# Optimization experiments

Measured on AMD Instinct MI355X. Metric: run time of the kernel, lower is better.

The kernel has to match this reference:

```python
import jax, jax.numpy as jnp
import numpy as np

H = 2048            # hidden_size
INTER = 8192        # intermediate_size
E = 16              # num_experts
V = 32000           # vocab_size
I = INTER // E      # per-expert intermediate (tp_size=1) = 512
N = 4096            # num_tokens
BASE_ROUTING_SCALE = 10.0


def setup_inputs() -> dict:
    key = jax.random.key(0)
    ks = jax.random.split(key, 6)
    x = jax.random.normal(ks[0], (N, H), dtype=jnp.float32)
    token_ids = jax.random.randint(ks[1], (N,), 0, V)
    mu = jax.random.normal(ks[2], (N, H), dtype=jnp.float32)
    # kaiming-uniform-ish scaled params
    gate_up_proj = jax.random.normal(ks[3], (E, H, 2 * I), dtype=jnp.float32) * (1.0 / np.sqrt(H))
    down_proj = jax.random.normal(ks[4], (E, I, H), dtype=jnp.float32) * (1.0 / np.sqrt(I))
    # mu_router initialized to zeros in the module; use small random so routing is actually mu-biased
    mu_router_w = jax.random.normal(ks[5], (E, H), dtype=jnp.float32) * 0.02
    return {"x": x, "token_ids": token_ids, "mu": mu,
            "gate_up_proj": gate_up_proj, "down_proj": down_proj,
            "mu_router_w": mu_router_w}


def reference(x, token_ids, mu, gate_up_proj, down_proj, mu_router_w):
    # --- routing: expert = token_id % E, biased by mu logits ---
    base = jnp.clip(token_ids, 0, V - 1) % E              # [N]
    logits = (jax.nn.one_hot(base, E, dtype=jnp.float32) * BASE_ROUTING_SCALE
              + mu @ mu_router_w.T)                       # [N, E]
    expert_ids = jnp.argmax(logits, axis=-1)              # [N]

    Iloc = gate_up_proj.shape[-1] // 2

    # --- grouped expert SwiGLU MLP: scan over experts, mask-combine outputs ---
    def step(acc, inp):
        wg, wd, e = inp
        gu = x @ wg                                       # [N, 2I]
        h = jax.nn.silu(gu[:, :Iloc]) * gu[:, Iloc:]      # [N, I]
        o = h @ wd                                        # [N, H]
        acc = acc + jnp.where((expert_ids == e)[:, None], o, 0.0)
        return acc, None

    out0 = jnp.zeros_like(x)
    out, _ = jax.lax.scan(step, out0, (gate_up_proj, down_proj, jnp.arange(E)))
    return out
```

## Files before the change

kernel.cpp:

```cpp
#include <hip/hip_runtime.h>
#include <hip/hip_bf16.h>

#define NT 4096
#define HD 2048
#define NE 16
#define ID 512
#define TWO_I 1024
#define PITCH 72
#define MAXITEMS 47

typedef __attribute__((ext_vector_type(8))) short bf16x8_t;
typedef __attribute__((ext_vector_type(4))) float f32x4_t;

__device__ __forceinline__ unsigned short f2bf(float f) {
  union { float f; unsigned int u; } v; v.f = f;
  unsigned int r = v.u + 0x7fffu + ((v.u >> 16) & 1u);
  return (unsigned short)(r >> 16);
}
__device__ __forceinline__ unsigned pk2(unsigned short a, unsigned short b) {
  return (unsigned)a | ((unsigned)b << 16);
}
__device__ __forceinline__ void gl_lds16(const void* g, void* l) {
  __builtin_amdgcn_global_load_lds(
      (const __attribute__((address_space(1))) unsigned int*)g,
      (__attribute__((address_space(3))) unsigned int*)l, 16, 0, 0);
}

__global__ void k_cast_x(const float* __restrict__ x, unsigned short* __restrict__ xb) {
  size_t i = ((size_t)blockIdx.x * 256 + threadIdx.x) * 8;
  float4 a = *(const float4*)(x + i);
  float4 b = *(const float4*)(x + i + 4);
  uint4 pk;
  pk.x = pk2(f2bf(a.x), f2bf(a.y)); pk.y = pk2(f2bf(a.z), f2bf(a.w));
  pk.z = pk2(f2bf(b.x), f2bf(b.y)); pk.w = pk2(f2bf(b.z), f2bf(b.w));
  *(uint4*)(xb + i) = pk;
}

__global__ void k_route(const float* __restrict__ mu, const int* __restrict__ tok,
                        const float* __restrict__ wr, int* __restrict__ eid) {
  int t = blockIdx.x;
  int tid = threadIdx.x;
  float p[NE];
#pragma unroll
  for (int e = 0; e < NE; ++e) p[e] = 0.f;
  const float* m = mu + (size_t)t * HD;
  for (int h = tid; h < HD; h += 256) {
    float mv = m[h];
#pragma unroll
    for (int e = 0; e < NE; ++e) p[e] += mv * wr[e * HD + h];
  }
#pragma unroll
  for (int e = 0; e < NE; ++e) {
    float v = p[e];
#pragma unroll
    for (int s = 32; s; s >>= 1) v += __shfl_xor(v, s, 64);
    p[e] = v;
  }
  __shared__ float red[4][NE];
  int lane = tid & 63, wv = tid >> 6;
  if (lane == 0) {
#pragma unroll
    for (int e = 0; e < NE; ++e) red[wv][e] = p[e];
  }
  __syncthreads();
  if (tid == 0) {
    int tk = tok[t];
    if (tk < 0) tk = 0;
    if (tk > 31999) tk = 31999;
    int base = tk & 15;
    float best = -3.0e38f; int bi = 0;
    for (int e = 0; e < NE; ++e) {
      float v = red[0][e] + red[1][e] + red[2][e] + red[3][e];
      if (e == base) v += 10.0f;
      if (v > best) { best = v; bi = e; }
    }
    eid[t] = bi;
  }
}

__global__ void k_init(int* counts, int* cursors) {
  int i = threadIdx.x;
  if (i < NE) { counts[i] = 0; cursors[i] = 0; }
}
__global__ void k_hist(const int* __restrict__ eid, int* __restrict__ counts) {
  int t = blockIdx.x * 256 + threadIdx.x;
  if (t < NT) atomicAdd(&counts[eid[t]], 1);
}
__global__ void k_scan(const int* __restrict__ counts, int* __restrict__ offsets,
                       int* __restrict__ cursors, int* __restrict__ wk) {
  if (threadIdx.x == 0) {
    int s = 0;
    for (int e = 0; e < NE; ++e) { offsets[e] = s; cursors[e] = s; s += counts[e]; }
    offsets[NE] = s;
    int n = 0;
    for (int e = 0; e < NE; ++e) {
      int tiles = (counts[e] + 127) >> 7;
      for (int m = 0; m < tiles; ++m) { wk[n++] = e | (m << 8); }
    }
    wk[MAXITEMS] = n;
  }
}
__global__ void k_scatter(const int* __restrict__ eid, int* __restrict__ cursors,
                          int* __restrict__ tlist) {
  int t = blockIdx.x * 256 + threadIdx.x;
  if (t < NT) {
    int e = eid[t];
    int pos = atomicAdd(&cursors[e], 1);
    tlist[pos] = t;
  }
}

__global__ __launch_bounds__(256, 3) void k_gemm1(
    const unsigned short* __restrict__ xb, const float* __restrict__ gup,
    const int* __restrict__ offsets, const int* __restrict__ tlist,
    const int* __restrict__ wk, unsigned short* __restrict__ hbuf) {
  int item = blockIdx.y;
  if (item >= wk[MAXITEMS]) return;
  int w = wk[item];
  int e = w & 255, tb = (w >> 8) * 128;
  int off = offsets[e], cnt = offsets[e + 1] - off;
  int c0 = blockIdx.x * 32;

  __shared__ float Bbuf[2][64 * 64];
  __shared__ unsigned short Pbuf[2][64 * PITCH];
  __shared__ int ltok[128];

  int tid = threadIdx.x, lane = tid & 63, wv = tid >> 6;
  if (tid < 128) { int r = tb + tid; if (r > cnt - 1) r = cnt - 1; ltok[tid] = tlist[off + r]; }
  __syncthreads();

  int lr = lane & 15, hi = lane >> 4, mb = wv * 32;
  const unsigned short* aRow0 = xb + (size_t)ltok[mb + lr] * HD + hi * 8;
  const unsigned short* aRow1 = xb + (size_t)ltok[mb + 16 + lr] * HD + hi * 8;

  const float* bSrc[4];
  int bDst[4];
  {
    int cc = lane & 15;
    int gcol = (cc < 8) ? (c0 + cc * 4) : (ID + c0 + (cc - 8) * 4);
    const float* Wg = gup + (size_t)e * HD * TWO_I;
#pragma unroll
    for (int i = 0; i < 4; ++i) {
      int kr = wv * 16 + i * 4 + (lane >> 4);
      bSrc[i] = Wg + (size_t)kr * TWO_I + gcol;
      bDst[i] = (wv * 16 + i * 4) * 64;
    }
  }

#define STAGEB(BUF) do { \
  _Pragma("unroll") for (int i = 0; i < 4; ++i) { \
    gl_lds16(bSrc[i], &Bbuf[BUF][bDst[i]]); bSrc[i] += (size_t)64 * TWO_I; } \
} while (0)

  bf16x8_t A0[4], A1[4];
#define LOADA(SET, KT) do { \
  SET[0] = *(const bf16x8_t*)(aRow0 + (KT) * 64); \
  SET[1] = *(const bf16x8_t*)(aRow0 + (KT) * 64 + 32); \
  SET[2] = *(const bf16x8_t*)(aRow1 + (KT) * 64); \
  SET[3] = *(const bf16x8_t*)(aRow1 + (KT) * 64 + 32); \
} while (0)

#define TRANSP(BUF) do { \
  const float* s_ = &Bbuf[BUF][(wv * 16) * 64 + lane]; \
  unsigned short t_[16]; \
  _Pragma("unroll") for (int j = 0; j < 16; ++j) t_[j] = f2bf(s_[j * 64]); \
  uint4 q0_, q1_; \
  q0_.x = pk2(t_[0], t_[1]);   q0_.y = pk2(t_[2], t_[3]); \
  q0_.z = pk2(t_[4], t_[5]);   q0_.w = pk2(t_[6], t_[7]); \
  q1_.x = pk2(t_[8], t_[9]);   q1_.y = pk2(t_[10], t_[11]); \
  q1_.z = pk2(t_[12], t_[13]); q1_.w = pk2(t_[14], t_[15]); \
  *(uint4*)&Pbuf[BUF][lane * PITCH + wv * 16] = q0_; \
  *(uint4*)&Pbuf[BUF][lane * PITCH + wv * 16 + 8] = q1_; \
} while (0)

  f32x4_t zero = {0.f, 0.f, 0.f, 0.f};
  f32x4_t accg[2][2], accu[2][2];
#pragma unroll
  for (int m = 0; m < 2; ++m)
#pragma unroll
    for (int n = 0; n < 2; ++n) { accg[m][n] = zero; accu[m][n] = zero; }

#define MFMA_PH(BUF, SET) do { \
  __builtin_amdgcn_s_setprio(1); \
  _Pragma("unroll") for (int kk = 0; kk < 2; ++kk) { \
    int klo = kk * 32 + hi * 8; \
    bf16x8_t bg0 = *(bf16x8_t*)&Pbuf[BUF][(lr) * PITCH + klo]; \
    bf16x8_t bg1 = *(bf16x8_t*)&Pbuf[BUF][(16 + lr) * PITCH + klo]; \
    bf16x8_t bu0 = *(bf16x8_t*)&Pbuf[BUF][(32 + lr) * PITCH + klo]; \
    bf16x8_t bu1 = *(bf16x8_t*)&Pbuf[BUF][(48 + lr) * PITCH + klo]; \
    bf16x8_t a0 = SET[kk], a1 = SET[2 + kk]; \
    accg[0][0] = __builtin_amdgcn_mfma_f32_16x16x32_bf16(a0, bg0, accg[0][0], 0, 0, 0); \
    accg[0][1] = __builtin_amdgcn_mfma_f32_16x16x32_bf16(a0, bg1, accg[0][1], 0, 0, 0); \
    accu[0][0] = __builtin_amdgcn_mfma_f32_16x16x32_bf16(a0, bu0, accu[0][0], 0, 0, 0); \
    accu[0][1] = __builtin_amdgcn_mfma_f32_16x16x32_bf16(a0, bu1, accu[0][1], 0, 0, 0); \
    accg[1][0] = __builtin_amdgcn_mfma_f32_16x16x32_bf16(a1, bg0, accg[1][0], 0, 0, 0); \
    accg[1][1] = __builtin_amdgcn_mfma_f32_16x16x32_bf16(a1, bg1, accg[1][1], 0, 0, 0); \
    accu[1][0] = __builtin_amdgcn_mfma_f32_16x16x32_bf16(a1, bu0, accu[1][0], 0, 0, 0); \
    accu[1][1] = __builtin_amdgcn_mfma_f32_16x16x32_bf16(a1, bu1, accu[1][1], 0, 0, 0); \
  } \
  __builtin_amdgcn_s_setprio(0); \
} while (0)

#define SUBSTEP(KT, BUF, SET, VMC) do { \
  asm volatile("s_waitcnt vmcnt(" #VMC ")" ::: "memory"); \
  __builtin_amdgcn_sched_barrier(0); \
  TRANSP(BUF); \
  asm volatile("s_waitcnt lgkmcnt(0)" ::: "memory"); \
  __builtin_amdgcn_sched_barrier(0); \
  __builtin_amdgcn_s_barrier(); \
  MFMA_PH(BUF, SET); \
  if ((KT) + 2 < 32) { LOADA(SET, (KT) + 2); STAGEB(BUF); } \
} while (0)

  LOADA(A0, 0); STAGEB(0);
  LOADA(A1, 1); STAGEB(1);

  for (int kt2 = 0; kt2 < 15; ++kt2) {
    SUBSTEP(2 * kt2, 0, A0, 8);
    SUBSTEP(2 * kt2 + 1, 1, A1, 8);
  }
  SUBSTEP(30, 0, A0, 8);
  SUBSTEP(31, 1, A1, 0);

#undef SUBSTEP
#undef MFMA_PH
#undef TRANSP
#undef LOADA
#undef STAGEB

  int rq = hi * 4;
#pragma unroll
  for (int m = 0; m < 2; ++m)
#pragma unroll
    for (int n = 0; n < 2; ++n)
#pragma unroll
      for (int j = 0; j < 4; ++j) {
        int r = tb + mb + m * 16 + rq + j;
        if (r < cnt) {
          float g = accg[m][n][j], u = accu[m][n][j];
          float hv = (g / (1.f + __expf(-g))) * u;
          hbuf[(size_t)(off + r) * ID + c0 + n * 16 + lr] = f2bf(hv);
        }
      }
}

__global__ __launch_bounds__(256, 3) void k_gemm2(
    const unsigned short* __restrict__ hbuf, const float* __restrict__ dwn,
    const int* __restrict__ offsets, const int* __restrict__ tlist,
    const int* __restrict__ wk, float* __restrict__ out) {
  int item = blockIdx.y;
  if (item >= wk[MAXITEMS]) return;
  int w = wk[item];
  int e = w & 255, tb = (w >> 8) * 128;
  int off = offsets[e], cnt = offsets[e + 1] - off;
  int c0 = blockIdx.x * 64;

  __shared__ float Bbuf[2][64 * 64];
  __shared__ unsigned short Pbuf[2][64 * PITCH];

  int tid = threadIdx.x, lane = tid & 63, wv = tid >> 6;
  int lr = lane & 15, hi = lane >> 4, mb = wv * 32;

  int r0 = tb + mb + lr;      if (r0 > cnt - 1) r0 = cnt - 1;
  int r1 = tb + mb + 16 + lr; if (r1 > cnt - 1) r1 = cnt - 1;
  const unsigned short* aRow0 = hbuf + (size_t)(off + r0) * ID + hi * 8;
  const unsigned short* aRow1 = hbuf + (size_t)(off + r1) * ID + hi * 8;

  const float* bSrc[4];
  int bDst[4];
  {
    int cc = lane & 15;
    const float* Wd = dwn + (size_t)e * ID * HD;
#pragma unroll
    for (int i = 0; i < 4; ++i) {
      int kr = wv * 16 + i * 4 + (lane >> 4);
      bSrc[i] = Wd + (size_t)kr * HD + c0 + cc * 4;
      bDst[i] = (wv * 16 + i * 4) * 64;
    }
  }

#define STAGEB(BUF) do { \
  _Pragma("unroll") for (int i = 0; i < 4; ++i) { \
    gl_lds16(bSrc[i], &Bbuf[BUF][bDst[i]]); bSrc[i] += (size_t)64 * HD; } \
} while (0)

  bf16x8_t A0[4], A1[4];
#define LOADA(SET, KT) do { \
  SET[0] = *(const bf16x8_t*)(aRow0 + (KT) * 64); \
  SET[1] = *(const bf16x8_t*)(aRow0 + (KT) * 64 + 32); \
  SET[2] = *(const bf16x8_t*)(aRow1 + (KT) * 64); \
  SET[3] = *(const bf16x8_t*)(aRow1 + (KT) * 64 + 32); \
} while (0)

#define TRANSP(BUF) do { \
  const float* s_ = &Bbuf[BUF][(wv * 16) * 64 + lane]; \
  unsigned short t_[16]; \
  _Pragma("unroll") for (int j = 0; j < 16; ++j) t_[j] = f2bf(s_[j * 64]); \
  uint4 q0_, q1_; \
  q0_.x = pk2(t_[0], t_[1]);   q0_.y = pk2(t_[2], t_[3]); \
  q0_.z = pk2(t_[4], t_[5]);   q0_.w = pk2(t_[6], t_[7]); \
  q1_.x = pk2(t_[8], t_[9]);   q1_.y = pk2(t_[10], t_[11]); \
  q1_.z = pk2(t_[12], t_[13]); q1_.w = pk2(t_[14], t_[15]); \
  *(uint4*)&Pbuf[BUF][lane * PITCH + wv * 16] = q0_; \
  *(uint4*)&Pbuf[BUF][lane * PITCH + wv * 16 + 8] = q1_; \
} while (0)

  f32x4_t zero = {0.f, 0.f, 0.f, 0.f};
  f32x4_t acc[2][4];
#pragma unroll
  for (int m = 0; m < 2; ++m)
#pragma unroll
    for (int n = 0; n < 4; ++n) acc[m][n] = zero;

#define MFMA_PH(BUF, SET) do { \
  __builtin_amdgcn_s_setprio(1); \
  _Pragma("unroll") for (int kk = 0; kk < 2; ++kk) { \
    int klo = kk * 32 + hi * 8; \
    bf16x8_t b0 = *(bf16x8_t*)&Pbuf[BUF][(lr) * PITCH + klo]; \
    bf16x8_t b1 = *(bf16x8_t*)&Pbuf[BUF][(16 + lr) * PITCH + klo]; \
    bf16x8_t b2 = *(bf16x8_t*)&Pbuf[BUF][(32 + lr) * PITCH + klo]; \
    bf16x8_t b3 = *(bf16x8_t*)&Pbuf[BUF][(48 + lr) * PITCH + klo]; \
    bf16x8_t a0 = SET[kk], a1 = SET[2 + kk]; \
    acc[0][0] = __builtin_amdgcn_mfma_f32_16x16x32_bf16(a0, b0, acc[0][0], 0, 0, 0); \
    acc[0][1] = __builtin_amdgcn_mfma_f32_16x16x32_bf16(a0, b1, acc[0][1], 0, 0, 0); \
    acc[0][2] = __builtin_amdgcn_mfma_f32_16x16x32_bf16(a0, b2, acc[0][2], 0, 0, 0); \
    acc[0][3] = __builtin_amdgcn_mfma_f32_16x16x32_bf16(a0, b3, acc[0][3], 0, 0, 0); \
    acc[1][0] = __builtin_amdgcn_mfma_f32_16x16x32_bf16(a1, b0, acc[1][0], 0, 0, 0); \
    acc[1][1] = __builtin_amdgcn_mfma_f32_16x16x32_bf16(a1, b1, acc[1][1], 0, 0, 0); \
    acc[1][2] = __builtin_amdgcn_mfma_f32_16x16x32_bf16(a1, b2, acc[1][2], 0, 0, 0); \
    acc[1][3] = __builtin_amdgcn_mfma_f32_16x16x32_bf16(a1, b3, acc[1][3], 0, 0, 0); \
  } \
  __builtin_amdgcn_s_setprio(0); \
} while (0)

#define SUBSTEP(KT, BUF, SET, VMC) do { \
  asm volatile("s_waitcnt vmcnt(" #VMC ")" ::: "memory"); \
  __builtin_amdgcn_sched_barrier(0); \
  TRANSP(BUF); \
  asm volatile("s_waitcnt lgkmcnt(0)" ::: "memory"); \
  __builtin_amdgcn_sched_barrier(0); \
  __builtin_amdgcn_s_barrier(); \
  MFMA_PH(BUF, SET); \
  if ((KT) + 2 < 8) { LOADA(SET, (KT) + 2); STAGEB(BUF); } \
} while (0)

  LOADA(A0, 0); STAGEB(0);
  LOADA(A1, 1); STAGEB(1);

  SUBSTEP(0, 0, A0, 8);
  SUBSTEP(1, 1, A1, 8);
  SUBSTEP(2, 0, A0, 8);
  SUBSTEP(3, 1, A1, 8);
  SUBSTEP(4, 0, A0, 8);
  SUBSTEP(5, 1, A1, 8);
  SUBSTEP(6, 0, A0, 8);
  SUBSTEP(7, 1, A1, 0);

#undef SUBSTEP
#undef MFMA_PH
#undef TRANSP
#undef LOADA
#undef STAGEB

  int rq = hi * 4;
#pragma unroll
  for (int m = 0; m < 2; ++m)
#pragma unroll
    for (int n = 0; n < 4; ++n)
#pragma unroll
      for (int j = 0; j < 4; ++j) {
        int r = tb + mb + m * 16 + rq + j;
        if (r < cnt) {
          out[(size_t)tlist[off + r] * HD + c0 + n * 16 + lr] = acc[m][n][j];
        }
      }
}

extern "C" void kernel_launch(void* const* d_in, const int* in_sizes, int n_in,
                              void* d_out, int out_size, void* d_ws, size_t ws_size,
                              hipStream_t stream) {
  (void)in_sizes; (void)n_in; (void)out_size; (void)ws_size;
  const float* x   = (const float*)d_in[0];
  const int*   tok = (const int*)d_in[1];
  const float* mu  = (const float*)d_in[2];
  const float* gup = (const float*)d_in[3];
  const float* dwn = (const float*)d_in[4];
  const float* wr  = (const float*)d_in[5];
  float* out = (float*)d_out;

  char* ws = (char*)d_ws;
  int* eid     = (int*)ws;
  int* tlist   = (int*)(ws + 16384);
  int* counts  = (int*)(ws + 32768);
  int* offsets = (int*)(ws + 32896);
  int* cursors = (int*)(ws + 33024);
  int* wk      = (int*)(ws + 33152);
  unsigned short* xb   = (unsigned short*)(ws + 65536);
  unsigned short* hbuf = (unsigned short*)(ws + 65536 + (size_t)NT * HD * 2);

  k_cast_x <<<4096, 256, 0, stream>>>(x, xb);
  k_route  <<<NT, 256, 0, stream>>>(mu, tok, wr, eid);
  k_init   <<<1, 64, 0, stream>>>(counts, cursors);
  k_hist   <<<16, 256, 0, stream>>>(eid, counts);
  k_scan   <<<1, 64, 0, stream>>>(counts, offsets, cursors, wk);
  k_scatter<<<16, 256, 0, stream>>>(eid, cursors, tlist);
  k_gemm1  <<<dim3(16, MAXITEMS), 256, 0, stream>>>(xb, gup, offsets, tlist, wk, hbuf);
  k_gemm2  <<<dim3(32, MAXITEMS), 256, 0, stream>>>(hbuf, dwn, offsets, tlist, wk, out);
}
```

Baseline: 201.3 us.

## Pre-cast expert weights to bf16 tiled layout and widen GEMM N-tiles

Adds per-call prep kernels that convert gate_up and down weights from fp32 into bf16 blocks of 64 columns, stored K-contiguous per expert. The GEMM kernels then stage bf16 tiles, which halves the bytes moved per tile and drops the fp32-to-bf16 conversion from the inner loop. Each block now covers twice as many output columns, with more accumulators and occupancy lowered to 2. The prep pass reads all fp32 weights and writes bf16 copies on every call, which adds a full weight-sized memory pass.

```diff
diff --git a/kernel.cpp b/kernel.cpp
--- a/kernel.cpp
+++ b/kernel.cpp
@@ -24,6 +24,38 @@
   __builtin_amdgcn_global_load_lds(
       (const __attribute__((address_space(1))) unsigned int*)g,
       (__attribute__((address_space(3))) unsigned int*)l, 16, 0, 0);
+}
+
+__global__ __launch_bounds__(256) void k_prep_gu(const float* __restrict__ gup,
+                                                 unsigned short* __restrict__ wgb) {
+  int e = blockIdx.y, k0 = blockIdx.x * 32;
+  int t = threadIdx.x;
+  int cb = t >> 4, c = (t & 15) * 4;
+  const float* src = gup + ((size_t)e * HD + k0) * TWO_I + t * 4;
+  unsigned short* dst = wgb + (((size_t)e * 16 + cb) * HD + k0) * 64 + c;
+#pragma unroll 4
+  for (int j = 0; j < 32; ++j) {
+    float4 v = *(const float4*)src; src += TWO_I;
+    uint2 p; p.x = pk2(f2bf(v.x), f2bf(v.y)); p.y = pk2(f2bf(v.z), f2bf(v.w));
+    *(uint2*)dst = p; dst += 64;
+  }
+}
+__global__ __launch_bounds__(256) void k_prep_dn(const float* __restrict__ dwn,
+                                                 unsigned short* __restrict__ wdb) {
+  int e = blockIdx.y, k0 = blockIdx.x * 32;
+  int t = threadIdx.x;
+  int cb = t >> 3, c = (t & 7) * 8;
+  const float* src = dwn + ((size_t)e * ID + k0) * HD + t * 8;
+  unsigned short* dst = wdb + (((size_t)e * 32 + cb) * ID + k0) * 64 + c;
+#pragma unroll 4
+  for (int j = 0; j < 32; ++j) {
+    float4 v0 = *(const float4*)src;
+    float4 v1 = *(const float4*)(src + 4); src += HD;
+    uint4 p;
+    p.x = pk2(f2bf(v0.x), f2bf(v0.y)); p.y = pk2(f2bf(v0.z), f2bf(v0.w));
+    p.z = pk2(f2bf(v1.x), f2bf(v1.y)); p.w = pk2(f2bf(v1.z), f2bf(v1.w));
+    *(uint4*)dst = p; dst += 64;
+  }
 }
 
 __global__ void k_cast_x(const float* __restrict__ x, unsigned short* __restrict__ xb) {
@@ -110,8 +142,8 @@
   }
 }
 
-__global__ __launch_bounds__(256, 3) void k_gemm1(
-    const unsigned short* __restrict__ xb, const float* __restrict__ gup,
+__global__ __launch_bounds__(256, 2) void k_gemm1(
+    const unsigned short* __restrict__ xb, const unsigned short* __restrict__ wgb,
     const int* __restrict__ offsets, const int* __restrict__ tlist,
     const int* __restrict__ wk, unsigned short* __restrict__ hbuf) {
   int item = blockIdx.y;
@@ -119,10 +151,11 @@
   int w = wk[item];
   int e = w & 255, tb = (w >> 8) * 128;
   int off = offsets[e], cnt = offsets[e + 1] - off;
-  int c0 = blockIdx.x * 32;
-
-  __shared__ float Bbuf[2][64 * 64];
-  __shared__ unsigned short Pbuf[2][64 * PITCH];
+  int cx = blockIdx.x;
+  int c0 = cx * 64;
+
+  __shared__ unsigned short Bb[2][2][64 * 64];
+  __shared__ unsigned short Pb[2][128 * PITCH];
   __shared__ int ltok[128];
 
   int tid = threadIdx.x, lane = tid & 63, wv = tid >> 6;
@@ -133,23 +166,23 @@
   const unsigned short* aRow0 = xb + (size_t)ltok[mb + lr] * HD + hi * 8;
   const unsigned short* aRow1 = xb + (size_t)ltok[mb + 16 + lr] * HD + hi * 8;
 
-  const float* bSrc[4];
-  int bDst[4];
+  const unsigned short* gS0;
+  const unsigned short* gS1;
+  const unsigned short* uS0;
+  const unsigned short* uS1;
   {
-    int cc = lane & 15;
-    int gcol = (cc < 8) ? (c0 + cc * 4) : (ID + c0 + (cc - 8) * 4);
-    const float* Wg = gup + (size_t)e * HD * TWO_I;
-#pragma unroll
-    for (int i = 0; i < 4; ++i) {
-      int kr = wv * 16 + i * 4 + (lane >> 4);
-      bSrc[i] = Wg + (size_t)kr * TWO_I + gcol;
-      bDst[i] = (wv * 16 + i * 4) * 64;
-    }
+    const unsigned short* gbase = wgb + ((size_t)(e * 16 + cx) * HD) * 64;
+    const unsigned short* ubase = wgb + ((size_t)(e * 16 + 8 + cx) * HD) * 64;
+    int lo = lane * 8;
+    gS0 = gbase + (wv * 16) * 64 + lo;      gS1 = gbase + (wv * 16 + 8) * 64 + lo;
+    uS0 = ubase + (wv * 16) * 64 + lo;      uS1 = ubase + (wv * 16 + 8) * 64 + lo;
   }
 
 #define STAGEB(BUF) do { \
-  _Pragma("unroll") for (int i = 0; i < 4; ++i) { \
-    gl_lds16(bSrc[i], &Bbuf[BUF][bDst[i]]); bSrc[i] += (size_t)64 * TWO_I; } \
+  gl_lds16(gS0, &Bb[BUF][0][(wv * 16) * 64]);     gS0 += 4096; \
+  gl_lds16(gS1, &Bb[BUF][0][(wv * 16 + 8) * 64]); gS1 += 4096; \
+  gl_lds16(uS0, &Bb[BUF][1][(wv * 16) * 64]);     uS0 += 4096; \
+  gl_lds16(uS1, &Bb[BUF][1][(wv * 16 + 8) * 64]); uS1 += 4096; \
 } while (0)
 
   bf16x8_t A0[4], A1[4];
@@ -161,42 +194,44 @@
 } while (0)
 
 #define TRANSP(BUF) do { \
-  const float* s_ = &Bbuf[BUF][(wv * 16) * 64 + lane]; \
-  unsigned short t_[16]; \
-  _Pragma("unroll") for (int j = 0; j < 16; ++j) t_[j] = f2bf(s_[j * 64]); \
-  uint4 q0_, q1_; \
-  q0_.x = pk2(t_[0], t_[1]);   q0_.y = pk2(t_[2], t_[3]); \
-  q0_.z = pk2(t_[4], t_[5]);   q0_.w = pk2(t_[6], t_[7]); \
-  q1_.x = pk2(t_[8], t_[9]);   q1_.y = pk2(t_[10], t_[11]); \
-  q1_.z = pk2(t_[12], t_[13]); q1_.w = pk2(t_[14], t_[15]); \
-  *(uint4*)&Pbuf[BUF][lane * PITCH + wv * 16] = q0_; \
-  *(uint4*)&Pbuf[BUF][lane * PITCH + wv * 16 + 8] = q1_; \
+  int T_ = lane >> 5, c2_ = (lane & 31) * 2; \
+  const unsigned short* b_ = &Bb[BUF][T_][(wv * 16) * 64 + c2_]; \
+  unsigned v_[16]; \
+  _Pragma("unroll") for (int j = 0; j < 16; ++j) v_[j] = *(const unsigned*)(b_ + j * 64); \
+  uint4 lo0_, lo1_, hi0_, hi1_; \
+  lo0_.x = (v_[0] & 0xffffu) | (v_[1] << 16);  lo0_.y = (v_[2] & 0xffffu) | (v_[3] << 16); \
+  lo0_.z = (v_[4] & 0xffffu) | (v_[5] << 16);  lo0_.w = (v_[6] & 0xffffu) | (v_[7] << 16); \
+  lo1_.x = (v_[8] & 0xffffu) | (v_[9] << 16);  lo1_.y = (v_[10] & 0xffffu) | (v_[11] << 16); \
+  lo1_.z = (v_[12] & 0xffffu) | (v_[13] << 16); lo1_.w = (v_[14] & 0xffffu) | (v_[15] << 16); \
+  hi0_.x = (v_[0] >> 16) | (v_[1] & 0xffff0000u);  hi0_.y = (v_[2] >> 16) | (v_[3] & 0xffff0000u); \
+  hi0_.z = (v_[4] >> 16) | (v_[5] & 0xffff0000u);  hi0_.w = (v_[6] >> 16) | (v_[7] & 0xffff0000u); \
+  hi1_.x = (v_[8] >> 16) | (v_[9] & 0xffff0000u);  hi1_.y = (v_[10] >> 16) | (v_[11] & 0xffff0000u); \
+  hi1_.z = (v_[12] >> 16) | (v_[13] & 0xffff0000u); hi1_.w = (v_[14] >> 16) | (v_[15] & 0xffff0000u); \
+  unsigned short* p0_ = &Pb[BUF][(T_ * 64 + c2_) * PITCH + wv * 16]; \
+  *(uint4*)p0_ = lo0_; *(uint4*)(p0_ + 8) = lo1_; \
+  *(uint4*)(p0_ + PITCH) = hi0_; *(uint4*)(p0_ + PITCH + 8) = hi1_; \
 } while (0)
 
   f32x4_t zero = {0.f, 0.f, 0.f, 0.f};
-  f32x4_t accg[2][2], accu[2][2];
+  f32x4_t accg[2][4], accu[2][4];
 #pragma unroll
   for (int m = 0; m < 2; ++m)
 #pragma unroll
-    for (int n = 0; n < 2; ++n) { accg[m][n] = zero; accu[m][n] = zero; }
+    for (int n = 0; n < 4; ++n) { accg[m][n] = zero; accu[m][n] = zero; }
 
 #define MFMA_PH(BUF, SET) do { \
   __builtin_amdgcn_s_setprio(1); \
   _Pragma("unroll") for (int kk = 0; kk < 2; ++kk) { \
     int klo = kk * 32 + hi * 8; \
-    bf16x8_t bg0 = *(bf16x8_t*)&Pbuf[BUF][(lr) * PITCH + klo]; \
-    bf16x8_t bg1 = *(bf16x8_t*)&Pbuf[BUF][(16 + lr) * PITCH + klo]; \
-    bf16x8_t bu0 = *(bf16x8_t*)&Pbuf[BUF][(32 + lr) * PITCH + klo]; \
-    bf16x8_t bu1 = *(bf16x8_t*)&Pbuf[BUF][(48 + lr) * PITCH + klo]; \
     bf16x8_t a0 = SET[kk], a1 = SET[2 + kk]; \
-    accg[0][0] = __builtin_amdgcn_mfma_f32_16x16x32_bf16(a0, bg0, accg[0][0], 0, 0, 0); \
-    accg[0][1] = __builtin_amdgcn_mfma_f32_16x16x32_bf16(a0, bg1, accg[0][1], 0, 0, 0); \
-    accu[0][0] = __builtin_amdgcn_mfma_f32_16x16x32_bf16(a0, bu0, accu[0][0], 0, 0, 0); \
-    accu[0][1] = __builtin_amdgcn_mfma_f32_16x16x32_bf16(a0, bu1, accu[0][1], 0, 0, 0); \
-    accg[1][0] = __builtin_amdgcn_mfma_f32_16x16x32_bf16(a1, bg0, accg[1][0], 0, 0, 0); \
-    accg[1][1] = __builtin_amdgcn_mfma_f32_16x16x32_bf16(a1, bg1, accg[1][1], 0, 0, 0); \
-    accu[1][0] = __builtin_amdgcn_mfma_f32_16x16x32_bf16(a1, bu0, accu[1][0], 0, 0, 0); \
-    accu[1][1] = __builtin_amdgcn_mfma_f32_16x16x32_bf16(a1, bu1, accu[1][1], 0, 0, 0); \
+    _Pragma("unroll") for (int n = 0; n < 4; ++n) { \
+      bf16x8_t bg = *(bf16x8_t*)&Pb[BUF][(n * 16 + lr) * PITCH + klo]; \
+      bf16x8_t bu = *(bf16x8_t*)&Pb[BUF][(64 + n * 16 + lr) * PITCH + klo]; \
+      accg[0][n] = __builtin_amdgcn_mfma_f32_16x16x32_bf16(a0, bg, accg[0][n], 0, 0, 0); \
+      accu[0][n] = __builtin_amdgcn_mfma_f32_16x16x32_bf16(a0, bu, accu[0][n], 0, 0, 0); \
+      accg[1][n] = __builtin_amdgcn_mfma_f32_16x16x32_bf16(a1, bg, accg[1][n], 0, 0, 0); \
+      accu[1][n] = __builtin_amdgcn_mfma_f32_16x16x32_bf16(a1, bu, accu[1][n], 0, 0, 0); \
+    } \
   } \
   __builtin_amdgcn_s_setprio(0); \
 } while (0)
@@ -232,7 +267,7 @@
 #pragma unroll
   for (int m = 0; m < 2; ++m)
 #pragma unroll
-    for (int n = 0; n < 2; ++n)
+    for (int n = 0; n < 4; ++n)
 #pragma unroll
       for (int j = 0; j < 4; ++j) {
         int r = tb + mb + m * 16 + rq + j;
@@ -244,8 +279,8 @@
       }
 }
 
-__global__ __launch_bounds__(256, 3) void k_gemm2(
-    const unsigned short* __restrict__ hbuf, const float* __restrict__ dwn,
+__global__ __launch_bounds__(256, 2) void k_gemm2(
+    const unsigned short* __restrict__ hbuf, const unsigned short* __restrict__ wdb,
     const int* __restrict__ offsets, const int* __restrict__ tlist,
     const int* __restrict__ wk, float* __restrict__ out) {
   int item = blockIdx.y;
@@ -253,10 +288,11 @@
   int w = wk[item];
   int e = w & 255, tb = (w >> 8) * 128;
   int off = offsets[e], cnt = offsets[e + 1] - off;
-  int c0 = blockIdx.x * 64;
-
-  __shared__ float Bbuf[2][64 * 64];
-  __shared__ unsigned short Pbuf[2][64 * PITCH];
+  int cx = blockIdx.x;
+  int c0 = cx * 128;
+
+  __shared__ unsigned short Bb[2][2][64 * 64];
+  __shared__ unsigned short Pb[2][128 * PITCH];
 
   int tid = threadIdx.x, lane = tid & 63, wv = tid >> 6;
   int lr = lane & 15, hi = lane >> 4, mb = wv * 32;
@@ -266,22 +302,23 @@
   const unsigned short* aRow0 = hbuf + (size_t)(off + r0) * ID + hi * 8;
   const unsigned short* aRow1 = hbuf + (size_t)(off + r1) * ID + hi * 8;
 
-  const float* bSrc[4];
-  int bDst[4];
+  const unsigned short* gS0;
+  const unsigned short* gS1;
+  const unsigned short* uS0;
+  const unsigned short* uS1;
   {
-    int cc = lane & 15;
-    const float* Wd = dwn + (size_t)e * ID * HD;
-#pragma unroll
-    for (int i = 0; i < 4; ++i) {
-      int kr = wv * 16 + i * 4 + (lane >> 4);
-      bSrc[i] = Wd + (size_t)kr * HD + c0 + cc * 4;
-      bDst[i] = (wv * 16 + i * 4) * 64;
-    }
+    const unsigned short* b0 = wdb + ((size_t)(e * 32 + 2 * cx) * ID) * 64;
+    const unsigned short* b1 = wdb + ((size_t)(e * 32 + 2 * cx + 1) * ID) * 64;
+    int lo = lane * 8;
+    gS0 = b0 + (wv * 16) * 64 + lo;  gS1 = b0 + (wv * 16 + 8) * 64 + lo;
+    uS0 = b1 + (wv * 16) * 64 + lo;  uS1 = b1 + (wv * 16 + 8) * 64 + lo;
   }
 
 #define STAGEB(BUF) do { \
-  _Pragma("unroll") for (int i = 0; i < 4; ++i) { \
-    gl_lds16(bSrc[i], &Bbuf[BUF][bDst[i]]); bSrc[i] += (size_t)64 * HD; } \
+  gl_lds16(gS0, &Bb[BUF][0][(wv * 16) * 64]);     gS0 += 4096; \
+  gl_lds16(gS1, &Bb[BUF][0][(wv * 16 + 8) * 64]); gS1 += 4096; \
+  gl_lds16(uS0, &Bb[BUF][1][(wv * 16) * 64]);     uS0 += 4096; \
+  gl_lds16(uS1, &Bb[BUF][1][(wv * 16 + 8) * 64]); uS1 += 4096; \
 } while (0)
 
   bf16x8_t A0[4], A1[4];
@@ -293,42 +330,41 @@
 } while (0)
 
 #define TRANSP(BUF) do { \
-  const float* s_ = &Bbuf[BUF][(wv * 16) * 64 + lane]; \
-  unsigned short t_[16]; \
-  _Pragma("unroll") for (int j = 0; j < 16; ++j) t_[j] = f2bf(s_[j * 64]); \
-  uint4 q0_, q1_; \
-  q0_.x = pk2(t_[0], t_[1]);   q0_.y = pk2(t_[2], t_[3]); \
-  q0_.z = pk2(t_[4], t_[5]);   q0_.w = pk2(t_[6], t_[7]); \
-  q1_.x = pk2(t_[8], t_[9]);   q1_.y = pk2(t_[10], t_[11]); \
-  q1_.z = pk2(t_[12], t_[13]); q1_.w = pk2(t_[14], t_[15]); \
-  *(uint4*)&Pbuf[BUF][lane * PITCH + wv * 16] = q0_; \
-  *(uint4*)&Pbuf[BUF][lane * PITCH + wv * 16 + 8] = q1_; \
+  int T_ = lane >> 5, c2_ = (lane & 31) * 2; \
+  const unsigned short* b_ = &Bb[BUF][T_][(wv * 16) * 64 + c2_]; \
+  unsigned v_[16]; \
+  _Pragma("unroll") for (int j = 0; j < 16; ++j) v_[j] = *(const unsigned*)(b_ + j * 64); \
+  uint4 lo0_, lo1_, hi0_, hi1_; \
+  lo0_.x = (v_[0] & 0xffffu) | (v_[1] << 16);  lo0_.y = (v_[2] & 0xffffu) | (v_[3] << 16); \
+  lo0_.z = (v_[4] & 0xffffu) | (v_[5] << 16);  lo0_.w = (v_[6] & 0xffffu) | (v_[7] << 16); \
+  lo1_.x = (v_[8] & 0xffffu) | (v_[9] << 16);  lo1_.y = (v_[10] & 0xffffu) | (v_[11] << 16); \
+  lo1_.z = (v_[12] & 0xffffu) | (v_[13] << 16); lo1_.w = (v_[14] & 0xffffu) | (v_[15] << 16); \
+  hi0_.x = (v_[0] >> 16) | (v_[1] & 0xffff0000u);  hi0_.y = (v_[2] >> 16) | (v_[3] & 0xffff0000u); \
+  hi0_.z = (v_[4] >> 16) | (v_[5] & 0xffff0000u);  hi0_.w = (v_[6] >> 16) | (v_[7] & 0xffff0000u); \
+  hi1_.x = (v_[8] >> 16) | (v_[9] & 0xffff0000u);  hi1_.y = (v_[10] >> 16) | (v_[11] & 0xffff0000u); \
+  hi1_.z = (v_[12] >> 16) | (v_[13] & 0xffff0000u); hi1_.w = (v_[14] >> 16) | (v_[15] & 0xffff0000u); \
+  unsigned short* p0_ = &Pb[BUF][(T_ * 64 + c2_) * PITCH + wv * 16]; \
+  *(uint4*)p0_ = lo0_; *(uint4*)(p0_ + 8) = lo1_; \
+  *(uint4*)(p0_ + PITCH) = hi0_; *(uint4*)(p0_ + PITCH + 8) = hi1_; \
 } while (0)
 
   f32x4_t zero = {0.f, 0.f, 0.f, 0.f};
-  f32x4_t acc[2][4];
+  f32x4_t acc[2][8];
 #pragma unroll
   for (int m = 0; m < 2; ++m)
 #pragma unroll
-    for (int n = 0; n < 4; ++n) acc[m][n] = zero;
+    for (int n = 0; n < 8; ++n) acc[m][n] = zero;
 
 #define MFMA_PH(BUF, SET) do { \
   __builtin_amdgcn_s_setprio(1); \
   _Pragma("unroll") for (int kk = 0; kk < 2; ++kk) { \
     int klo = kk * 32 + hi * 8; \
-    bf16x8_t b0 = *(bf16x8_t*)&Pbuf[BUF][(lr) * PITCH + klo]; \
-    bf16x8_t b1 = *(bf16x8_t*)&Pbuf[BUF][(16 + lr) * PITCH + klo]; \
-    bf16x8_t b2 = *(bf16x8_t*)&Pbuf[BUF][(32 + lr) * PITCH + klo]; \
-    bf16x8_t b3 = *(bf16x8_t*)&Pbuf[BUF][(48 + lr) * PITCH + klo]; \
     bf16x8_t a0 = SET[kk], a1 = SET[2 + kk]; \
-    acc[0][0] = __builtin_amdgcn_mfma_f32_16x16x32_bf16(a0, b0, acc[0][0], 0, 0, 0); \
-    acc[0][1] = __builtin_amdgcn_mfma_f32_16x16x32_bf16(a0, b1, acc[0][1], 0, 0, 0); \
-    acc[0][2] = __builtin_amdgcn_mfma_f32_16x16x32_bf16(a0, b2, acc[0][2], 0, 0, 0); \
-    acc[0][3] = __builtin_amdgcn_mfma_f32_16x16x32_bf16(a0, b3, acc[0][3], 0, 0, 0); \
-    acc[1][0] = __builtin_amdgcn_mfma_f32_16x16x32_bf16(a1, b0, acc[1][0], 0, 0, 0); \
-    acc[1][1] = __builtin_amdgcn_mfma_f32_16x16x32_bf16(a1, b1, acc[1][1], 0, 0, 0); \
-    acc[1][2] = __builtin_amdgcn_mfma_f32_16x16x32_bf16(a1, b2, acc[1][2], 0, 0, 0); \
-    acc[1][3] = __builtin_amdgcn_mfma_f32_16x16x32_bf16(a1, b3, acc[1][3], 0, 0, 0); \
+    _Pragma("unroll") for (int n = 0; n < 8; ++n) { \
+      bf16x8_t b = *(bf16x8_t*)&Pb[BUF][(n * 16 + lr) * PITCH + klo]; \
+      acc[0][n] = __builtin_amdgcn_mfma_f32_16x16x32_bf16(a0, b, acc[0][n], 0, 0, 0); \
+      acc[1][n] = __builtin_amdgcn_mfma_f32_16x16x32_bf16(a1, b, acc[1][n], 0, 0, 0); \
+    } \
   } \
   __builtin_amdgcn_s_setprio(0); \
 } while (0)
@@ -366,7 +402,7 @@
 #pragma unroll
   for (int m = 0; m < 2; ++m)
 #pragma unroll
-    for (int n = 0; n < 4; ++n)
+    for (int n = 0; n < 8; ++n)
 #pragma unroll
       for (int j = 0; j < 4; ++j) {
         int r = tb + mb + m * 16 + rq + j;
@@ -396,14 +432,18 @@
   int* cursors = (int*)(ws + 33024);
   int* wk      = (int*)(ws + 33152);
   unsigned short* xb   = (unsigned short*)(ws + 65536);
-  unsigned short* hbuf = (unsigned short*)(ws + 65536 + (size_t)NT * HD * 2);
-
+  unsigned short* hbuf = (unsigned short*)(ws + 65536 + 16777216);
+  unsigned short* wgb  = (unsigned short*)(ws + 65536 + 16777216 + 4194304);
+  unsigned short* wdb  = (unsigned short*)(ws + 65536 + 16777216 + 4194304 + 67108864);
+
+  k_prep_gu<<<dim3(64, 16), 256, 0, stream>>>(gup, wgb);
+  k_prep_dn<<<dim3(16, 16), 256, 0, stream>>>(dwn, wdb);
   k_cast_x <<<4096, 256, 0, stream>>>(x, xb);
   k_route  <<<NT, 256, 0, stream>>>(mu, tok, wr, eid);
   k_init   <<<1, 64, 0, stream>>>(counts, cursors);
   k_hist   <<<16, 256, 0, stream>>>(eid, counts);
   k_scan   <<<1, 64, 0, stream>>>(counts, offsets, cursors, wk);
   k_scatter<<<16, 256, 0, stream>>>(eid, cursors, tlist);
-  k_gemm1  <<<dim3(16, MAXITEMS), 256, 0, stream>>>(xb, gup, offsets, tlist, wk, hbuf);
-  k_gemm2  <<<dim3(32, MAXITEMS), 256, 0, stream>>>(hbuf, dwn, offsets, tlist, wk, out);
-}
+  k_gemm1  <<<dim3(8, MAXITEMS), 256, 0, stream>>>(xb, wgb, offsets, tlist, wk, hbuf);
+  k_gemm2  <<<dim3(16, MAXITEMS), 256, 0, stream>>>(hbuf, wdb, offsets, tlist, wk, out);
+}
```

Result: slower. 234.3 us (+16.4%).
